# Optimization experiments

Hardware: AMD Instinct MI355X
Metric: run time of the kernel (lower is better)

Reference implementation:

```python
import jax, jax.numpy as jnp
import numpy as np
import math

N, HID, H = 20000, 128, 8
C = HID // H  # out_channels per head = 16
E = 640000


def setup_inputs() -> dict:
    key = jax.random.key(0)
    ks = jax.random.split(key, 16)
    s = 0.08  # weight init scale (~kaiming for fan_in 128)
    inp = {
        "h": jax.random.normal(ks[0], (N, HID), dtype=jnp.float32),
        "vec": jax.random.normal(ks[1], (N, 3, HID), dtype=jnp.float32),
        "edge_index": jax.random.randint(ks[2], (2, E), 0, N, dtype=jnp.int64),
        # weights stored as [in, out] (x @ W + b)
        "Wq": jax.random.normal(ks[3], (HID, H * C), dtype=jnp.float32) * s,
        "bq": jax.random.normal(ks[4], (H * C,), dtype=jnp.float32) * s,
        "Wk": jax.random.normal(ks[5], (HID, H * C), dtype=jnp.float32) * s,
        "bk": jax.random.normal(ks[6], (H * C,), dtype=jnp.float32) * s,
        "Wv": jax.random.normal(ks[7], (HID, H * C * 2), dtype=jnp.float32) * s,
        "bv": jax.random.normal(ks[8], (H * C * 2,), dtype=jnp.float32) * s,
        "Wp": jax.random.normal(ks[9], (C, C * 3), dtype=jnp.float32) * 0.2,
        "bp": jax.random.normal(ks[10], (C * 3,), dtype=jnp.float32) * 0.2,
        "Wvec": jax.random.normal(ks[11], (H * C, H * C * 3), dtype=jnp.float32) * s,
    }
    return inp


def reference(h, vec, edge_index, Wq, bq, Wk, bk, Wv, bv, Wp, bp, Wvec):
    n = h.shape[0]
    query = (h @ Wq + bq).reshape(n, H, C)                      # [N,H,C]
    vp = (vec @ Wvec).reshape(n, 3, H, 3, C)                    # vec_proj, no bias
    vec1, vec2, vec3 = vp[:, :, :, 0], vp[:, :, :, 1], vp[:, :, :, 2]  # [N,3,H,C]
    vec_hc = vec.reshape(n, 3, H, C)
    vec_dot = (vec1 * vec2).sum(axis=1)                         # [N,H,C]

    src, dst = edge_index[0], edge_index[1]  # j (source), i (target)
    xj = h[src]                                                 # [E,HID] gather
    k_ij = (xj @ Wk + bk).reshape(-1, H, C)                     # [E,H,C]
    v_ij = (xj @ Wv + bv).reshape(-1, H, 2, C)                  # [E,H,2,C]
    alpha = (query[dst] * k_ij).sum(-1) / math.sqrt(C)          # [E,H]

    # segment softmax over edges grouped by destination node
    amax = jax.ops.segment_max(alpha, dst, num_segments=n)      # [N,H]
    ex = jnp.exp(alpha - amax[dst])
    denom = jax.ops.segment_sum(ex, dst, num_segments=n)
    alpha = ex / denom[dst]                                     # [E,H]

    h_msg, s1 = v_ij[:, :, 0], v_ij[:, :, 1]                    # [E,H,C] each
    msg = h_msg * alpha[..., None]                              # [E,H,C]
    vmsg = vec_hc[src] * s1[:, None]                            # [E,3,H,C]

    out_x = jax.ops.segment_sum(msg, dst, num_segments=n)       # [N,H,C]
    vec_agg = jax.ops.segment_sum(vmsg, dst, num_segments=n)    # [N,3,H,C]

    qp = (out_x.reshape(n * H, C) @ Wp + bp).reshape(n, H, 3, C)
    q1, q2, q3 = qp[:, :, 0], qp[:, :, 1], qp[:, :, 2]          # [N,H,C]
    dx = (q2 + q3 * vec_dot).reshape(n, H * C)
    dvec = (vec3 * q1[:, None] + vec_agg).reshape(n, 3, H * C)
    return (h + dx, vec + dvec)
```

## Files before the change

kernel.cpp:

```cpp
#include <hip/hip_runtime.h>
#include <hip/hip_bf16.h>
#include <math.h>


typedef __attribute__((ext_vector_type(8))) short bf16x8;
typedef __attribute__((ext_vector_type(4))) float f32x4;

#define ROWB 656
#define PADDEG 96

static __device__ inline unsigned f2bf(float x) {
    union { float f; unsigned u; } v; v.f = x;
    return (v.u + 0x7FFFu + ((v.u >> 16) & 1u)) >> 16;
}
static __device__ inline unsigned pack2(float a, float b) {
    return f2bf(a) | (f2bf(b) << 16);
}
static __device__ inline float bflo(unsigned w) {
    union { unsigned u; float f; } v; v.u = w << 16; return v.f;
}
static __device__ inline float bfhi(unsigned w) {
    union { unsigned u; float f; } v; v.u = w & 0xFFFF0000u; return v.f;
}
static __device__ inline unsigned qb(float x) {
    return (unsigned)(__float2int_rn(x) + 128);
}
#define UB(w, i) ((float)(((w) >> (8 * (i))) & 0xffu))

__global__ __launch_bounds__(256) void prep_kernel(
    const float* __restrict__ Wq, const float* __restrict__ Wk,
    const float* __restrict__ Wv, const float* __restrict__ Wvec,
    const float* __restrict__ bq, const float* __restrict__ bk,
    const float* __restrict__ bv,
    unsigned short* __restrict__ WBT, unsigned short* __restrict__ WVT,
    float* __restrict__ biasAll, int* __restrict__ deg, int n) {
    int idx = blockIdx.x * 256 + threadIdx.x;
    if (idx < 512 * 128) {
        int c = idx >> 7, k = idx & 127;
        float v;
        if (c < 128) v = Wq[k * 128 + c];
        else if (c < 256) v = Wk[k * 128 + (c - 128)];
        else v = Wv[k * 256 + (c - 256)];
        WBT[(k >> 5) * (512 * 32) + c * 32 + (k & 31)] = (unsigned short)f2bf(v);
    } else if (idx < 512 * 128 + 384 * 128) {
        int j = idx - 512 * 128;
        int c = j >> 7, k = j & 127;
        WVT[(k >> 5) * (384 * 32) + c * 32 + (k & 31)] = (unsigned short)f2bf(Wvec[k * 384 + c]);
    } else if (idx < 512 * 128 + 384 * 128 + 512) {
        int c = idx - (512 * 128 + 384 * 128);
        biasAll[c] = (c < 128) ? bq[c] : (c < 256) ? bk[c - 128] : bv[c - 256];
    } else {
        int j = idx - (512 * 128 + 384 * 128 + 512);
        if (j < n) deg[j] = 0;
    }
}

static __device__ void gemm_body(const float* __restrict__ A,
                                 const unsigned short* __restrict__ BT,
                                 const float* __restrict__ bias,
                                 float* __restrict__ C,
                                 unsigned short* __restrict__ Cb,
                                 int M, int ldc, int ncols,
                                 int bx, int by) {
    __shared__ unsigned short sA[64 * 40];
    __shared__ unsigned short sB[128 * 40];
    int tid = threadIdx.x;
    int row0 = bx * 64, col0 = by * 128;
    int wid = tid >> 6, lane = tid & 63;
    int wr = (wid >> 1) * 32, wc = (wid & 1) * 64;
    int lr = lane & 15, lk = lane >> 4;
    f32x4 acc[2][4] = {};
#pragma unroll
    for (int ks = 0; ks < 4; ++ks) {
        if (ks) __syncthreads();
        {
            int r = tid >> 2, kk = (tid & 3) * 8;
            uint4 w = make_uint4(0u, 0u, 0u, 0u);
            int grow = row0 + r;
            if (grow < M) {
                const float* ap = &A[(size_t)grow * 128 + ks * 32 + kk];
                float4 x0 = *(const float4*)ap;
                float4 x1 = *(const float4*)(ap + 4);
                w.x = pack2(x0.x, x0.y); w.y = pack2(x0.z, x0.w);
                w.z = pack2(x1.x, x1.y); w.w = pack2(x1.z, x1.w);
            }
            *(uint4*)&sA[r * 40 + kk] = w;
        }
        {
            int c = tid >> 1, off16 = (tid & 1) * 16;
            const unsigned short* bp = BT + (size_t)ks * ncols * 32 +
                                       (size_t)(col0 + c) * 32 + off16;
            uint4 wb0 = *(const uint4*)bp;
            uint4 wb1 = *(const uint4*)(bp + 8);
            *(uint4*)&sB[c * 40 + off16] = wb0;
            *(uint4*)&sB[c * 40 + off16 + 8] = wb1;
        }
        __syncthreads();
        bf16x8 af[2], bfr[4];
#pragma unroll
        for (int mm = 0; mm < 2; ++mm)
            af[mm] = *(const bf16x8*)&sA[(wr + mm * 16 + lr) * 40 + lk * 8];
#pragma unroll
        for (int nn = 0; nn < 4; ++nn)
            bfr[nn] = *(const bf16x8*)&sB[(wc + nn * 16 + lr) * 40 + lk * 8];
#pragma unroll
        for (int mm = 0; mm < 2; ++mm)
#pragma unroll
            for (int nn = 0; nn < 4; ++nn)
                acc[mm][nn] = __builtin_amdgcn_mfma_f32_16x16x32_bf16(af[mm], bfr[nn],
                                                                     acc[mm][nn], 0, 0, 0);
    }
#pragma unroll
    for (int mm = 0; mm < 2; ++mm) {
#pragma unroll
        for (int r4 = 0; r4 < 4; ++r4) {
            int row = row0 + wr + mm * 16 + lk * 4 + r4;
            if (row >= M) continue;
#pragma unroll
            for (int nn = 0; nn < 4; ++nn) {
                int col = col0 + wc + nn * 16 + lr;
                float v = acc[mm][nn][r4];
                if (bias) v += bias[col];
                if (Cb) Cb[(size_t)row * ldc + col] = (unsigned short)f2bf(v);
                else C[(size_t)row * ldc + col] = v;
            }
        }
    }
}

__global__ __launch_bounds__(256) void scatter_gemm_kernel(
    const int* __restrict__ ei, int* __restrict__ deg, int* __restrict__ padcol, int E,
    const float* __restrict__ hin, const unsigned short* __restrict__ WBT,
    const float* __restrict__ biasAll, float* __restrict__ Cqkv, int M, int nbxQ,
    const float* __restrict__ vec, const unsigned short* __restrict__ WVT,
    unsigned short* __restrict__ Cvp, int Mv, int nbxV,
    int scatBlocks, int qkvBlocks) {
    if (blockIdx.x < (unsigned)scatBlocks) {
        int i4 = (blockIdx.x * 256 + threadIdx.x) * 4;
        if (i4 + 3 < E) {
            int4 s4 = *(const int4*)&ei[i4];
            int4 d4 = *(const int4*)&ei[E + i4];
            int p0 = atomicAdd(&deg[d4.x], 1);
            if (p0 < PADDEG) padcol[d4.x * PADDEG + p0] = s4.x;
            int p1 = atomicAdd(&deg[d4.y], 1);
            if (p1 < PADDEG) padcol[d4.y * PADDEG + p1] = s4.y;
            int p2 = atomicAdd(&deg[d4.z], 1);
            if (p2 < PADDEG) padcol[d4.z * PADDEG + p2] = s4.z;
            int p3 = atomicAdd(&deg[d4.w], 1);
            if (p3 < PADDEG) padcol[d4.w * PADDEG + p3] = s4.w;
        } else {
            for (int i = i4; i < E; ++i) {
                int dd = ei[E + i];
                int p = atomicAdd(&deg[dd], 1);
                if (p < PADDEG) padcol[dd * PADDEG + p] = ei[i];
            }
        }
        return;
    }
    int b = blockIdx.x - scatBlocks;
    if (b < qkvBlocks) {
        gemm_body(hin, WBT, biasAll, Cqkv, (unsigned short*)nullptr, M, 512, 512,
                  b % nbxQ, b / nbxQ);
    } else {
        b -= qkvBlocks;
        gemm_body(vec, WVT, (const float*)nullptr, (float*)nullptr, Cvp, Mv, 384, 384,
                  b % nbxV, b / nbxV);
    }
}

__global__ __launch_bounds__(256) void pack_kernel(const float* __restrict__ Cqkv,
                                                   const float* __restrict__ vec,
                                                   char* __restrict__ nodeP, int n) {
    int lane = threadIdx.x & 63;
    int node = blockIdx.x * 4 + (threadIdx.x >> 6);
    if (node >= n) return;
    int hc0 = lane * 2, hh = lane >> 3, c0 = hc0 & 15;
    const float* row = &Cqkv[(size_t)node * 512];
    float2 kk = *(const float2*)&row[128 + hc0];
    float2 v0 = *(const float2*)&row[256 + hh * 32 + c0];
    float2 s1 = *(const float2*)&row[256 + hh * 32 + 16 + c0];
    float2 a0 = *(const float2*)&vec[(size_t)node * 384 + 0 * 128 + hc0];
    float2 a1 = *(const float2*)&vec[(size_t)node * 384 + 1 * 128 + hc0];
    float2 a2 = *(const float2*)&vec[(size_t)node * 384 + 2 * 128 + hc0];
    float f00 = a0.x * s1.x, f01 = a0.y * s1.y;
    float f10 = a1.x * s1.x, f11 = a1.y * s1.y;
    float f20 = a2.x * s1.x, f21 = a2.y * s1.y;
    float km = fmaxf(fabsf(kk.x), fabsf(kk.y));
    float vm = fmaxf(fabsf(v0.x), fabsf(v0.y));
    float fm = fmaxf(fmaxf(fmaxf(fabsf(f00), fabsf(f01)), fmaxf(fabsf(f10), fabsf(f11))),
                     fmaxf(fabsf(f20), fabsf(f21)));
#pragma unroll
    for (int off = 1; off < 64; off <<= 1) {
        km = fmaxf(km, __shfl_xor(km, off, 64));
        vm = fmaxf(vm, __shfl_xor(vm, off, 64));
        fm = fmaxf(fm, __shfl_xor(fm, off, 64));
    }
    km = fmaxf(km, 1e-20f);
    vm = fmaxf(vm, 1e-20f);
    fm = fmaxf(fm, 1e-20f);
    float ki = 127.f / km, vi = 127.f / vm, fi = 127.f / fm;
    unsigned kvw = qb(kk.x * ki) | (qb(kk.y * ki) << 8) | (qb(v0.x * vi) << 16) |
                   (qb(v0.y * vi) << 24);
    unsigned fAw = qb(f00 * fi) | (qb(f01 * fi) << 8) | (qb(f10 * fi) << 16) |
                   (qb(f11 * fi) << 24);
    unsigned short fCw = (unsigned short)(qb(f20 * fi) | (qb(f21 * fi) << 8));
    char* rp = nodeP + (size_t)node * ROWB;
    *(uint2*)(rp + 16 + lane * 8) = make_uint2(kvw, fAw);
    *(unsigned short*)(rp + 528 + lane * 2) = fCw;
    if (lane == 0)
        *(float4*)rp = make_float4(km * (0.25f * 1.44269504088896f / 127.f),
                                   vm * (1.f / 127.f), fm * (1.f / 127.f), 0.f);
}

__global__ __launch_bounds__(256) void agg_kernel(
    const int* __restrict__ deg, const int* __restrict__ padcol,
    const float* __restrict__ Cqkv, const unsigned short* __restrict__ Cvp,
    const char* __restrict__ nodeP,
    const float* __restrict__ hin, const float* __restrict__ vecin,
    const float* __restrict__ Wp, const float* __restrict__ bp,
    float* __restrict__ out0, float* __restrict__ out1, int n) {
    __shared__ float sWp[768];
    __shared__ float sbp[48];
    for (int i = threadIdx.x; i < 768; i += 256) sWp[i] = Wp[i];
    for (int i = threadIdx.x; i < 48; i += 256) sbp[i] = bp[i];
    __syncthreads();
    int lane = threadIdx.x & 63;
    int node = blockIdx.x * 4 + (threadIdx.x >> 6);
    if (node >= n) return;
    int cnt = deg[node];
    if (cnt > PADDEG) cnt = PADDEG;
    int hc0 = lane * 2;
    int hh = lane >> 3, c0 = hc0 & 15;
    int off8 = 16 + lane * 8;
    int off2 = 528 + lane * 2;
    float2 qv = *(const float2*)&Cqkv[(size_t)node * 512 + hc0];
    float qs = qv.x + qv.y;
    qs += __shfl_xor(qs, 1, 64);
    qs += __shfl_xor(qs, 2, 64);
    qs += __shfl_xor(qs, 4, 64);
    float c0q = 128.f * qs;
    float d = 0.f, ha0 = 0.f, ha1 = 0.f, esum = 0.f, fsS = 0.f;
    float va[6] = {0.f, 0.f, 0.f, 0.f, 0.f, 0.f};
    {
        int myc = (lane < cnt) ? padcol[node * PADDEG + lane] : 0;
        int myc2 = (64 + lane < cnt) ? padcol[node * PADDEG + 64 + lane] : 0;
        int e = 0;
        for (; e + 7 < cnt; e += 8) {
            uint2 kw[8]; unsigned fC[8]; float4 sc4[8];
#pragma unroll
            for (int u = 0; u < 8; ++u) {
                int ee = e + u;
                int s = (ee < 64) ? __builtin_amdgcn_readlane(myc, ee)
                                  : __builtin_amdgcn_readlane(myc2, ee - 64);
                const char* rb = nodeP + (size_t)(unsigned)s * ROWB;
                sc4[u] = *(const float4*)rb;
                kw[u] = *(const uint2*)(rb + off8);
                fC[u] = *(const unsigned short*)(rb + off2);
            }
#pragma unroll
            for (int u = 0; u < 8; ++u) {
                float t = qv.x * UB(kw[u].x, 0) + qv.y * UB(kw[u].x, 1);
                t += __shfl_xor(t, 1, 64);
                t += __shfl_xor(t, 2, 64);
                t += __shfl_xor(t, 4, 64);
                float ew = exp2f(sc4[u].x * (t - c0q));
                d += ew;
                float evs = ew * sc4[u].y;
                esum += evs;
                ha0 += evs * UB(kw[u].x, 2);
                ha1 += evs * UB(kw[u].x, 3);
                float fs = sc4[u].z;
                va[0] += fs * UB(kw[u].y, 0);
                va[1] += fs * UB(kw[u].y, 1);
                va[2] += fs * UB(kw[u].y, 2);
                va[3] += fs * UB(kw[u].y, 3);
                va[4] += fs * UB(fC[u], 0);
                va[5] += fs * UB(fC[u], 1);
                fsS += fs;
            }
        }
        for (; e < cnt; ++e) {
            int s = (e < 64) ? __builtin_amdgcn_readlane(myc, e)
                             : __builtin_amdgcn_readlane(myc2, e - 64);
            const char* rb = nodeP + (size_t)(unsigned)s * ROWB;
            float4 sc4 = *(const float4*)rb;
            uint2 kw = *(const uint2*)(rb + off8);
            unsigned fC = *(const unsigned short*)(rb + off2);
            float t = qv.x * UB(kw.x, 0) + qv.y * UB(kw.x, 1);
            t += __shfl_xor(t, 1, 64);
            t += __shfl_xor(t, 2, 64);
            t += __shfl_xor(t, 4, 64);
            float ew = exp2f(sc4.x * (t - c0q));
            d += ew;
            float evs = ew * sc4.y;
            esum += evs;
            ha0 += evs * UB(kw.x, 2);
            ha1 += evs * UB(kw.x, 3);
            float fs = sc4.z;
            va[0] += fs * UB(kw.y, 0);
            va[1] += fs * UB(kw.y, 1);
            va[2] += fs * UB(kw.y, 2);
            va[3] += fs * UB(kw.y, 3);
            va[4] += fs * UB(fC, 0);
            va[5] += fs * UB(fC, 1);
            fsS += fs;
        }
    }
    float inv = (d > 0.f) ? 1.f / d : 0.f;
    float corr = 128.f * esum;
    float ox0 = (ha0 - corr) * inv, ox1 = (ha1 - corr) * inv;
    float fcor = 128.f * fsS;
#pragma unroll
    for (int j = 0; j < 6; ++j) va[j] -= fcor;
    int cc0 = (lane & 7) * 2;
    float accq[6];
#pragma unroll
    for (int jj = 0; jj < 6; jj++) {
        int j = jj >> 1, c = cc0 + (jj & 1);
        accq[jj] = sbp[j * 16 + c];
    }
#pragma unroll
    for (int cp = 0; cp < 16; cp++) {
        int srcLane = (lane & 56) | (cp >> 1);
        float val = __shfl((cp & 1) ? ox1 : ox0, srcLane, 64);
#pragma unroll
        for (int jj = 0; jj < 6; jj++) {
            int j = jj >> 1, c = cc0 + (jj & 1);
            accq[jj] += val * sWp[cp * 48 + j * 16 + c];
        }
    }
    float2 vd2 = make_float2(0.f, 0.f);
#pragma unroll
    for (int s3 = 0; s3 < 3; s3++) {
        size_t vbase = ((size_t)node * 3 + s3) * 384 + hh * 48;
        unsigned w1 = *(const unsigned*)&Cvp[vbase + c0];
        unsigned w2 = *(const unsigned*)&Cvp[vbase + 16 + c0];
        vd2.x += bflo(w1) * bflo(w2);
        vd2.y += bfhi(w1) * bfhi(w2);
    }
    float2 hv = *(const float2*)&hin[(size_t)node * 128 + hc0];
    float2 o0;
    o0.x = hv.x + accq[2] + accq[4] * vd2.x;
    o0.y = hv.y + accq[3] + accq[5] * vd2.y;
    *(float2*)&out0[(size_t)node * 128 + hc0] = o0;
#pragma unroll
    for (int s3 = 0; s3 < 3; s3++) {
        unsigned w3 = *(const unsigned*)&Cvp[((size_t)node * 3 + s3) * 384 + hh * 48 + 32 + c0];
        float2 vv = *(const float2*)&vecin[(size_t)node * 384 + s3 * 128 + hc0];
        float2 o1;
        o1.x = vv.x + bflo(w3) * accq[0] + va[s3 * 2 + 0];
        o1.y = vv.y + bfhi(w3) * accq[1] + va[s3 * 2 + 1];
        *(float2*)&out1[(size_t)node * 384 + s3 * 128 + hc0] = o1;
    }
}

extern "C" void kernel_launch(void* const* d_in, const int* in_sizes, int n_in,
                              void* d_out, int out_size, void* d_ws, size_t ws_size,
                              hipStream_t stream) {
    const float* hin = (const float*)d_in[0];
    const float* vec = (const float*)d_in[1];
    const int* ei = (const int*)d_in[2];
    const float* Wq = (const float*)d_in[3];
    const float* bq = (const float*)d_in[4];
    const float* Wk = (const float*)d_in[5];
    const float* bk = (const float*)d_in[6];
    const float* Wv = (const float*)d_in[7];
    const float* bv = (const float*)d_in[8];
    const float* Wp = (const float*)d_in[9];
    const float* bp = (const float*)d_in[10];
    const float* Wvec = (const float*)d_in[11];

    int N = in_sizes[0] / 128;
    int E = in_sizes[2] / 2;
    float* out0 = (float*)d_out;
    float* out1 = out0 + (size_t)N * 128;

    float* wsf = (float*)d_ws;
    size_t off = 0;
    float* Cqkv = wsf + off; off += (size_t)N * 512;
    unsigned short* Cvp = (unsigned short*)(wsf + off); off += (size_t)N * 576;
    char* nodeP = (char*)(wsf + off); off += ((size_t)N * ROWB + 3) / 4;
    unsigned short* WBT = (unsigned short*)(wsf + off); off += (size_t)512 * 128 / 2;
    unsigned short* WVT = (unsigned short*)(wsf + off); off += (size_t)384 * 128 / 2;
    float* biasAll = wsf + off; off += 512;
    int* ip = (int*)(wsf + off);
    int* deg = ip;            ip += N;
    int* padcol = ip;         ip += (size_t)N * PADDEG;

    int prepWork = 512 * 128 + 384 * 128 + 512 + N;
    hipLaunchKernelGGL(prep_kernel, dim3((prepWork + 255) / 256), dim3(256), 0, stream,
                       Wq, Wk, Wv, Wvec, bq, bk, bv, WBT, WVT, biasAll, deg, N);

    int scatBlocks = (E / 4 + 255) / 256;
    int nbxQ = (N + 63) / 64;
    int qkvBlocks = nbxQ * 4;
    int nbxV = (3 * N + 63) / 64;
    int vecBlocks = nbxV * 3;
    hipLaunchKernelGGL(scatter_gemm_kernel, dim3(scatBlocks + qkvBlocks + vecBlocks),
                       dim3(256), 0, stream,
                       ei, deg, padcol, E, hin, WBT, biasAll, Cqkv, N, nbxQ,
                       vec, WVT, Cvp, 3 * N, nbxV, scatBlocks, qkvBlocks);

    hipLaunchKernelGGL(pack_kernel, dim3((N + 3) / 4), dim3(256), 0, stream,
                       Cqkv, vec, nodeP, N);

    hipLaunchKernelGGL(agg_kernel, dim3((N + 3) / 4), dim3(256), 0, stream,
                       deg, padcol, Cqkv, Cvp, nodeP, hin, vec, Wp, bp, out0, out1, N);
}
```

Baseline: 174.8 us.

## Prefetch GEMM tiles into registers and interleave scatter blocks with GEMM blocks

The GEMM k-loop now loads the next k-slice of A and B into registers while the MFMA work on the current slice runs, so global-load latency overlaps compute. The block-to-work mapping also changes: one scatter (atomic degree/adjacency build) block is placed after every six GEMM blocks instead of all scatter blocks running first. The aim is to spread atomic-heavy memory traffic alongside MFMA work across the GPU. The cost is extra registers for the prefetch buffers and slightly more complex block indexing.

```diff
diff --git a/kernel.cpp b/kernel.cpp
--- a/kernel.cpp
+++ b/kernel.cpp
@@ -69,33 +69,44 @@
     int wid = tid >> 6, lane = tid & 63;
     int wr = (wid >> 1) * 32, wc = (wid & 1) * 64;
     int lr = lane & 15, lk = lane >> 4;
+    int rA = tid >> 2, kkA = (tid & 3) * 8;
+    int cB = tid >> 1, oB = (tid & 1) * 16;
+    int growA = row0 + rA;
+    bool aok = growA < M;
+    const float* apBase = &A[(size_t)growA * 128 + kkA];
+    const unsigned short* bpBase = BT + (size_t)(col0 + cB) * 32 + oB;
     f32x4 acc[2][4] = {};
+    uint4 wa, wb0, wb1;
+    {
+        wa = make_uint4(0u, 0u, 0u, 0u);
+        if (aok) {
+            float4 x0 = *(const float4*)apBase;
+            float4 x1 = *(const float4*)(apBase + 4);
+            wa.x = pack2(x0.x, x0.y); wa.y = pack2(x0.z, x0.w);
+            wa.z = pack2(x1.x, x1.y); wa.w = pack2(x1.z, x1.w);
+        }
+        wb0 = *(const uint4*)bpBase;
+        wb1 = *(const uint4*)(bpBase + 8);
+    }
 #pragma unroll
     for (int ks = 0; ks < 4; ++ks) {
-        if (ks) __syncthreads();
-        {
-            int r = tid >> 2, kk = (tid & 3) * 8;
-            uint4 w = make_uint4(0u, 0u, 0u, 0u);
-            int grow = row0 + r;
-            if (grow < M) {
-                const float* ap = &A[(size_t)grow * 128 + ks * 32 + kk];
+        *(uint4*)&sA[rA * 40 + kkA] = wa;
+        *(uint4*)&sB[cB * 40 + oB] = wb0;
+        *(uint4*)&sB[cB * 40 + oB + 8] = wb1;
+        __syncthreads();
+        if (ks < 3) {
+            wa = make_uint4(0u, 0u, 0u, 0u);
+            if (aok) {
+                const float* ap = apBase + (ks + 1) * 32;
                 float4 x0 = *(const float4*)ap;
                 float4 x1 = *(const float4*)(ap + 4);
-                w.x = pack2(x0.x, x0.y); w.y = pack2(x0.z, x0.w);
-                w.z = pack2(x1.x, x1.y); w.w = pack2(x1.z, x1.w);
+                wa.x = pack2(x0.x, x0.y); wa.y = pack2(x0.z, x0.w);
+                wa.z = pack2(x1.x, x1.y); wa.w = pack2(x1.z, x1.w);
             }
-            *(uint4*)&sA[r * 40 + kk] = w;
-        }
-        {
-            int c = tid >> 1, off16 = (tid & 1) * 16;
-            const unsigned short* bp = BT + (size_t)ks * ncols * 32 +
-                                       (size_t)(col0 + c) * 32 + off16;
-            uint4 wb0 = *(const uint4*)bp;
-            uint4 wb1 = *(const uint4*)(bp + 8);
-            *(uint4*)&sB[c * 40 + off16] = wb0;
-            *(uint4*)&sB[c * 40 + off16 + 8] = wb1;
-        }
-        __syncthreads();
+            const unsigned short* bp = bpBase + (size_t)(ks + 1) * ncols * 32;
+            wb0 = *(const uint4*)bp;
+            wb1 = *(const uint4*)(bp + 8);
+        }
         bf16x8 af[2], bfr[4];
 #pragma unroll
         for (int mm = 0; mm < 2; ++mm)
@@ -109,6 +120,7 @@
             for (int nn = 0; nn < 4; ++nn)
                 acc[mm][nn] = __builtin_amdgcn_mfma_f32_16x16x32_bf16(af[mm], bfr[nn],
                                                                      acc[mm][nn], 0, 0, 0);
+        if (ks < 3) __syncthreads();
     }
 #pragma unroll
     for (int mm = 0; mm < 2; ++mm) {
@@ -128,43 +140,57 @@
     }
 }
 
+static __device__ void scatter_body(const int* __restrict__ ei, int* __restrict__ deg,
+                                    int* __restrict__ padcol, int E, int g) {
+    int i4 = (g * 256 + threadIdx.x) * 4;
+    if (i4 + 3 < E) {
+        int4 s4 = *(const int4*)&ei[i4];
+        int4 d4 = *(const int4*)&ei[E + i4];
+        int p0 = atomicAdd(&deg[d4.x], 1);
+        if (p0 < PADDEG) padcol[d4.x * PADDEG + p0] = s4.x;
+        int p1 = atomicAdd(&deg[d4.y], 1);
+        if (p1 < PADDEG) padcol[d4.y * PADDEG + p1] = s4.y;
+        int p2 = atomicAdd(&deg[d4.z], 1);
+        if (p2 < PADDEG) padcol[d4.z * PADDEG + p2] = s4.z;
+        int p3 = atomicAdd(&deg[d4.w], 1);
+        if (p3 < PADDEG) padcol[d4.w * PADDEG + p3] = s4.w;
+    } else {
+        for (int i = i4; i < E; ++i) {
+            int dd = ei[E + i];
+            int p = atomicAdd(&deg[dd], 1);
+            if (p < PADDEG) padcol[dd * PADDEG + p] = ei[i];
+        }
+    }
+}
+
 __global__ __launch_bounds__(256) void scatter_gemm_kernel(
     const int* __restrict__ ei, int* __restrict__ deg, int* __restrict__ padcol, int E,
     const float* __restrict__ hin, const unsigned short* __restrict__ WBT,
     const float* __restrict__ biasAll, float* __restrict__ Cqkv, int M, int nbxQ,
     const float* __restrict__ vec, const unsigned short* __restrict__ WVT,
     unsigned short* __restrict__ Cvp, int Mv, int nbxV,
-    int scatBlocks, int qkvBlocks) {
-    if (blockIdx.x < (unsigned)scatBlocks) {
-        int i4 = (blockIdx.x * 256 + threadIdx.x) * 4;
-        if (i4 + 3 < E) {
-            int4 s4 = *(const int4*)&ei[i4];
-            int4 d4 = *(const int4*)&ei[E + i4];
-            int p0 = atomicAdd(&deg[d4.x], 1);
-            if (p0 < PADDEG) padcol[d4.x * PADDEG + p0] = s4.x;
-            int p1 = atomicAdd(&deg[d4.y], 1);
-            if (p1 < PADDEG) padcol[d4.y * PADDEG + p1] = s4.y;
-            int p2 = atomicAdd(&deg[d4.z], 1);
-            if (p2 < PADDEG) padcol[d4.z * PADDEG + p2] = s4.z;
-            int p3 = atomicAdd(&deg[d4.w], 1);
-            if (p3 < PADDEG) padcol[d4.w * PADDEG + p3] = s4.w;
+    int scatBlocks, int qkvBlocks, int ilv) {
+    int b = blockIdx.x;
+    int gemmIdx;
+    if (ilv) {
+        if (b < 7 * scatBlocks) {
+            int g = b / 7, slot = b - g * 7;
+            if (slot == 0) { scatter_body(ei, deg, padcol, E, g); return; }
+            gemmIdx = b - g - 1;
         } else {
-            for (int i = i4; i < E; ++i) {
-                int dd = ei[E + i];
-                int p = atomicAdd(&deg[dd], 1);
-                if (p < PADDEG) padcol[dd * PADDEG + p] = ei[i];
-            }
-        }
-        return;
-    }
-    int b = blockIdx.x - scatBlocks;
-    if (b < qkvBlocks) {
+            gemmIdx = b - scatBlocks;
+        }
+    } else {
+        if (b < scatBlocks) { scatter_body(ei, deg, padcol, E, b); return; }
+        gemmIdx = b - scatBlocks;
+    }
+    if (gemmIdx < qkvBlocks) {
         gemm_body(hin, WBT, biasAll, Cqkv, (unsigned short*)nullptr, M, 512, 512,
-                  b % nbxQ, b / nbxQ);
+                  gemmIdx % nbxQ, gemmIdx / nbxQ);
     } else {
-        b -= qkvBlocks;
+        gemmIdx -= qkvBlocks;
         gemm_body(vec, WVT, (const float*)nullptr, (float*)nullptr, Cvp, Mv, 384, 384,
-                  b % nbxV, b / nbxV);
+                  gemmIdx % nbxV, gemmIdx / nbxV);
     }
 }
 
@@ -396,10 +422,12 @@
     int qkvBlocks = nbxQ * 4;
     int nbxV = (3 * N + 63) / 64;
     int vecBlocks = nbxV * 3;
-    hipLaunchKernelGGL(scatter_gemm_kernel, dim3(scatBlocks + qkvBlocks + vecBlocks),
+    int gemmBlocks = qkvBlocks + vecBlocks;
+    int ilv = (gemmBlocks >= 6 * scatBlocks) ? 1 : 0;
+    hipLaunchKernelGGL(scatter_gemm_kernel, dim3(scatBlocks + gemmBlocks),
                        dim3(256), 0, stream,
                        ei, deg, padcol, E, hin, WBT, biasAll, Cqkv, N, nbxQ,
-                       vec, WVT, Cvp, 3 * N, nbxV, scatBlocks, qkvBlocks);
+                       vec, WVT, Cvp, 3 * N, nbxV, scatBlocks, qkvBlocks, ilv);
 
     hipLaunchKernelGGL(pack_kernel, dim3((N + 3) / 4), dim3(256), 0, stream,
                        Cqkv, vec, nodeP, N);
```

Result: faster. 156.9 us (-10.2%).
